# Optimization experiments

Measured on AMD Instinct MI355X. Metric: run time of the kernel, lower is better.

## Reference

```python
import jax, jax.numpy as jnp
import numpy as np

EPS = 1e-5
GROUPS = 16


def _deform_conv_gn(input, offset, mask, weight, bias, gamma, beta):
    # Modulated deformable conv v2 (k=3, stride=1, pad=1) + GroupNorm(16).
    B, C, H, W = input.shape
    Co = weight.shape[0]
    K = 9
    # kernel taps relative to center (pad=1 cancels the -1 origin shift)
    ky = jnp.repeat(jnp.arange(3) - 1, 3).astype(input.dtype)   # [9]
    kx = jnp.tile(jnp.arange(3) - 1, 3).astype(input.dtype)     # [9]
    off = offset.reshape(B, K, 2, H, W)                          # (dy, dx) per tap
    dy, dx = off[:, :, 0], off[:, :, 1]                          # [B,9,H,W]
    y = jnp.arange(H, dtype=input.dtype)[None, None, :, None] + ky[None, :, None, None] + dy
    x = jnp.arange(W, dtype=input.dtype)[None, None, None, :] + kx[None, :, None, None] + dx
    y0 = jnp.floor(y)
    x0 = jnp.floor(x)
    flat = input.reshape(B, C, H * W)

    def corner(yc, xc):
        # zero-padded bilinear corner gather -> [B,C,9,H,W]
        valid = ((yc >= 0) & (yc < H) & (xc >= 0) & (xc < W)).astype(input.dtype)
        yi = jnp.clip(yc, 0, H - 1).astype(jnp.int32)
        xi = jnp.clip(xc, 0, W - 1).astype(jnp.int32)
        idx = (yi * W + xi).reshape(B, -1)
        g = jax.vmap(lambda im, ix: jnp.take(im, ix, axis=1))(flat, idx)
        return g.reshape(B, C, K, H, W) * valid[:, None]

    wy1 = y - y0
    wx1 = x - x0
    wy0 = 1.0 - wy1
    wx0 = 1.0 - wx1
    val = (corner(y0, x0) * (wy0 * wx0)[:, None]
           + corner(y0, x0 + 1.0) * (wy0 * wx1)[:, None]
           + corner(y0 + 1.0, x0) * (wy1 * wx0)[:, None]
           + corner(y0 + 1.0, x0 + 1.0) * (wy1 * wx1)[:, None])
    cols = val * mask[:, None]                                   # modulation [B,C,9,H,W]
    out = jnp.einsum('bckhw,ock->bohw', cols, weight.reshape(Co, C, K))
    out = out + bias[None, :, None, None]
    # GroupNorm(16)
    g = out.reshape(B, GROUPS, Co // GROUPS, H, W)
    mu = g.mean(axis=(2, 3, 4), keepdims=True)
    var = g.var(axis=(2, 3, 4), keepdims=True)
    g = (g - mu) * jax.lax.rsqrt(var + EPS)
    return g.reshape(B, Co, H, W) * gamma[None, :, None, None] + beta[None, :, None, None]


def setup_inputs() -> dict:
    key = jax.random.key(0)
    k1, k2, k3, k4 = jax.random.split(key, 4)
    B, C, Co, H, W = 4, 256, 256, 64, 64
    return {
        'input': jax.random.normal(k1, (B, C, H, W), dtype=jnp.float32),
        'offset': jax.random.normal(k2, (B, 18, H, W), dtype=jnp.float32),
        'mask': jax.random.uniform(k3, (B, 9, H, W), dtype=jnp.float32),
        'weight': jax.random.normal(k4, (Co, C, 3, 3), dtype=jnp.float32) * 0.02,
        'bias': jnp.zeros((Co,), dtype=jnp.float32),
        'gamma': jnp.ones((Co,), dtype=jnp.float32),
        'beta': jnp.zeros((Co,), dtype=jnp.float32),
    }


def reference(input, offset, mask, weight, bias, gamma, beta):
    return _deform_conv_gn(input, offset, mask, weight, bias, gamma, beta)
```

## Files before the change

kernel.cpp:

```cpp
#include <hip/hip_runtime.h>

typedef __attribute__((ext_vector_type(8))) short short8;
typedef __attribute__((ext_vector_type(4))) float f32x4;

#define Bsz 4
#define Cin 256
#define Cout 256
#define Hh 64
#define Ww 64
#define HW 4096
#define NG 16
#define EPSV 1e-5f

#define CSTR 40
#define SPAN 16
#define PLF (SPAN*64)

#define OFF_IN   0
#define SZ_IN    (32 * PLF * 4)
#define OFF_COL  (OFF_IN + SZ_IN)
#define SZ_COL   (2 * 64 * CSTR * 2)
#define OFF_TA   (OFF_COL + SZ_COL)
#define SZ_TA    (576 * 8)
#define OFF_TW   (OFF_TA + SZ_TA)
#define SZ_TW    (576 * 16)
#define OFF_CTL  (OFF_TW + SZ_TW)
#define SMEM_BYTES (OFF_CTL + 16)

static __device__ __forceinline__ unsigned f2bf(float f) {
    unsigned u = __float_as_uint(f);
    return (u + 0x7fffu + ((u >> 16) & 1u)) >> 16;
}

static __device__ __forceinline__ float2 ld8(const float* p) {
    float2 v;
    __builtin_memcpy(&v, p, 8);
    return v;
}

__global__ void wt_kernel(const float* __restrict__ w, ushort* __restrict__ wtb,
                          float* __restrict__ stats) {
    const int i = blockIdx.x * 256 + threadIdx.x;
    if (blockIdx.x == 0 && threadIdx.x < 128) stats[threadIdx.x] = 0.f;
    if (i >= 72 * 256 * 32) return;
    const int cl = i & 31;
    const int o  = (i >> 5) & 255;
    const int ks = i >> 13;
    const int c  = ((ks & 7) << 5) | cl;
    const int kk = ks >> 3;
    wtb[i] = (ushort)f2bf(w[((size_t)o * Cin + c) * 9 + kk]);
}

__launch_bounds__(512, 1)
__global__ void dcn_kernel(const float* __restrict__ in,
                           const float* __restrict__ offs,
                           const float* __restrict__ mask,
                           const ushort* __restrict__ wtb,
                           const float* __restrict__ bias,
                           float* __restrict__ out,
                           float* __restrict__ stats) {
    extern __shared__ char smem[];
    float*  s_in = (float*)(smem + OFF_IN);
    ushort* col  = (ushort*)(smem + OFF_COL);
    int2*   s_ta = (int2*)(smem + OFF_TA);
    float4* s_tw = (float4*)(smem + OFF_TW);
    int*    s_ctl = (int*)(smem + OFF_CTL);

    const int t  = threadIdx.x;
    const int bx = blockIdx.x;
    const int q  = bx & 7, r = bx >> 3;
    const int b  = q >> 1;
    const int h  = ((q & 1) << 5) | r;
    const int lane = t & 63;
    const int wv   = t >> 6;
    const int n    = lane;
    const int quad = lane >> 4;
    const int l15  = lane & 15;

    if (t < 2) s_ctl[t] = (t == 0) ? 64 : -1;
    __syncthreads();

    int my_min = 64, my_max = -1;
    for (int j = t; j < 576; j += 512) {
        const int k = j >> 6, pp = j & 63;
        const float* ob = offs + (size_t)b * 18 * HW + h * Ww + pp;
        const float dy = ob[(2 * k) * HW];
        const float dx = ob[(2 * k + 1) * HW];
        const float m  = mask[((size_t)b * 9 + k) * HW + h * Ww + pp];
        const float y = (float)h + (float)(k / 3 - 1) + dy;
        const float x = (float)pp + (float)(k % 3 - 1) + dx;
        const float y0f = floorf(y), x0f = floorf(x);
        const float ly = y - y0f, lx = x - x0f;
        const float hy = 1.f - ly, hx = 1.f - lx;
        const int y0 = (int)y0f, x0 = (int)x0f;
        const int yc0 = min(max(y0, 0), 63);
        const int yc1 = min(max(y0 + 1, 0), 63);
        const int xb  = min(max(x0, 0), 62);
        float ax = 0.f, ay = 0.f;
        if (x0 == xb) {
            ax = hx;
            ay = lx;
        } else if (x0 < xb) {
            ax = (x0 + 1 == 0) ? lx : 0.f;
        } else {
            ay = (x0 == 63) ? hx : 0.f;
        }
        const float w0 = (y0 >= 0 && y0 < 64) ? m * hy : 0.f;
        const float w1 = (y0 + 1 >= 0 && y0 + 1 < 64) ? m * ly : 0.f;
        s_ta[j] = make_int2(yc0 * 64 + xb, yc1 * 64 + xb);
        s_tw[j] = make_float4(w0 * ax, w0 * ay, w1 * ax, w1 * ay);
        my_min = min(my_min, yc0);
        my_max = max(my_max, yc1);
    }
#pragma unroll
    for (int off = 32; off; off >>= 1) {
        my_min = min(my_min, __shfl_xor(my_min, off));
        my_max = max(my_max, __shfl_xor(my_max, off));
    }
    if (lane == 0) {
        atomicMin(&s_ctl[0], my_min);
        atomicMax(&s_ctl[1], my_max);
    }
    __syncthreads();

    const int ymin = s_ctl[0];
    const bool use_lds = (s_ctl[1] - ymin + 1) <= SPAN;
    const int ymin64 = ymin << 6;

    f32x4 acc[2][4];
#pragma unroll
    for (int i = 0; i < 2; i++)
#pragma unroll
        for (int nt = 0; nt < 4; nt++) acc[i][nt] = (f32x4){0.f, 0.f, 0.f, 0.f};

    const float* inb = in + (size_t)b * Cin * HW;

#define STAGE(cc)                                                              \
    {                                                                          \
        const float* cbs = inb + (size_t)((cc) * 32) * HW;                     \
        _Pragma("unroll")                                                      \
        for (int i = 0; i < 16; i++) {                                         \
            const int g = (wv << 4) | i;                                       \
            const int plane = g >> 2;                                          \
            const int row = min(ymin + ((g & 3) << 2) + (lane >> 4), 63);      \
            const float* src = cbs + (size_t)plane * HW + row * 64 +           \
                               ((lane & 15) << 2);                             \
            __builtin_amdgcn_global_load_lds(                                  \
                (const __attribute__((address_space(1))) void*)src,            \
                (__attribute__((address_space(3))) void*)(smem + OFF_IN +      \
                                                          g * 1024),          \
                16, 0, 0);                                                     \
        }                                                                      \
    }

#define GATHER_L(kk, pk0, pk1)                                             \
    {                                                                      \
        const int2  ad = s_ta[(kk) * 64 + n];                              \
        const float4 tw = s_tw[(kk) * 64 + n];                             \
        const int r0 = ad.x - ymin64, r1 = ad.y - ymin64;                  \
        const float* cb = s_in + (wv << 2) * PLF;                          \
        float vv[4];                                                       \
        _Pragma("unroll")                                                  \
        for (int j = 0; j < 4; j++) {                                      \
            const float* pl = cb + j * PLF;                                \
            const float2 g0 = ld8(pl + r0);                                \
            const float2 g1 = ld8(pl + r1);                                \
            vv[j] = tw.x * g0.x + tw.y * g0.y + tw.z * g1.x + tw.w * g1.y; \
        }                                                                  \
        pk0 = f2bf(vv[0]) | (f2bf(vv[1]) << 16);                           \
        pk1 = f2bf(vv[2]) | (f2bf(vv[3]) << 16);                           \
    }

#define GATHER_G(cc, kk, pk0, pk1)                                         \
    {                                                                      \
        const int2  ad = s_ta[(kk) * 64 + n];                              \
        const float4 tw = s_tw[(kk) * 64 + n];                             \
        const float* cb = inb + (size_t)((cc) * 32 + wv * 4) * HW;         \
        float vv[4];                                                       \
        _Pragma("unroll")                                                  \
        for (int j = 0; j < 4; j++) {                                      \
            const float* pl = cb + j * HW;                                 \
            const float2 g0 = ld8(pl + ad.x);                              \
            const float2 g1 = ld8(pl + ad.y);                              \
            vv[j] = tw.x * g0.x + tw.y * g0.y + tw.z * g1.x + tw.w * g1.y; \
        }                                                                  \
        pk0 = f2bf(vv[0]) | (f2bf(vv[1]) << 16);                           \
        pk1 = f2bf(vv[2]) | (f2bf(vv[3]) << 16);                           \
    }

#define FRAGS_MFMA(ks, p)                                                      \
    {                                                                          \
        const ushort* wp =                                                     \
            wtb + ((size_t)((ks) * 256 + wv * 32 + l15)) * 32 + quad * 8;      \
        const short8 a0 = *(const short8*)wp;                                  \
        const short8 a1 = *(const short8*)(wp + 16 * 32);                      \
        short8 bfr[4];                                                         \
        _Pragma("unroll")                                                      \
        for (int nt = 0; nt < 4; nt++)                                         \
            bfr[nt] = *(const short8*)&col[(p) * (64 * CSTR) +                 \
                                           (nt * 16 + l15) * CSTR + quad * 8]; \
        _Pragma("unroll")                                                      \
        for (int nt = 0; nt < 4; nt++) {                                       \
            acc[0][nt] = __builtin_amdgcn_mfma_f32_16x16x32_bf16(              \
                a0, bfr[nt], acc[0][nt], 0, 0, 0);                             \
            acc[1][nt] = __builtin_amdgcn_mfma_f32_16x16x32_bf16(              \
                a1, bfr[nt], acc[1][nt], 0, 0, 0);                             \
        }                                                                      \
    }

    unsigned pk0, pk1;
    int p = 0;

    if (use_lds) {
        STAGE(0);
        __syncthreads();
        GATHER_L(0, pk0, pk1);
#pragma unroll 1
        for (int s = 0; s < 72; s++) {
            const int cc = s / 9;
            const int kk = s - cc * 9;
            const int ks = kk * 8 + cc;
            *(unsigned long long*)&col[p * (64 * CSTR) + n * CSTR + (wv << 2)] =
                (unsigned long long)pk0 | ((unsigned long long)pk1 << 32);
            __syncthreads();
            const bool bound = (kk == 8) && (s != 71);
            if (bound) {
                STAGE(cc + 1);
            } else if (s != 71) {
                GATHER_L(kk + 1, pk0, pk1);
            }
            FRAGS_MFMA(ks, p);
            if (bound) {
                __syncthreads();
                GATHER_L(0, pk0, pk1);
            }
            p ^= 1;
        }
    } else {
        GATHER_G(0, 0, pk0, pk1);
#pragma unroll 1
        for (int s = 0; s < 72; s++) {
            const int cc = s / 9;
            const int kk = s - cc * 9;
            const int ks = kk * 8 + cc;
            *(unsigned long long*)&col[p * (64 * CSTR) + n * CSTR + (wv << 2)] =
                (unsigned long long)pk0 | ((unsigned long long)pk1 << 32);
            __syncthreads();
            if (s < 71) {
                const int s1 = s + 1;
                const int cc1 = s1 / 9;
                GATHER_G(cc1, s1 - cc1 * 9, pk0, pk1);
            }
            FRAGS_MFMA(ks, p);
            p ^= 1;
        }
    }
#undef STAGE
#undef GATHER_L
#undef GATHER_G
#undef FRAGS_MFMA

    float gs[2], gq[2];
#pragma unroll
    for (int i = 0; i < 2; i++) {
        float s = 0.f, qq = 0.f;
        const int ob = wv * 32 + i * 16 + quad * 4;
#pragma unroll
        for (int reg = 0; reg < 4; reg++) {
            const int o = ob + reg;
            const float bv = bias[o];
            float* op = out + ((size_t)(b * 256 + o)) * HW + h * Ww + l15;
#pragma unroll
            for (int nt = 0; nt < 4; nt++) {
                const float v = acc[i][nt][reg] + bv;
                op[nt * 16] = v;
                s += v;
                qq += v * v;
            }
        }
        gs[i] = s; gq[i] = qq;
    }
#pragma unroll
    for (int off = 32; off; off >>= 1) {
        gs[0] += __shfl_xor(gs[0], off);
        gq[0] += __shfl_xor(gq[0], off);
        gs[1] += __shfl_xor(gs[1], off);
        gq[1] += __shfl_xor(gq[1], off);
    }
    if (lane == 0) {
#pragma unroll
        for (int i = 0; i < 2; i++) {
            const int g = wv * 2 + i;
            atomicAdd(&stats[((size_t)b * NG + g) * 2],     gs[i]);
            atomicAdd(&stats[((size_t)b * NG + g) * 2 + 1], gq[i]);
        }
    }
}

__global__ void gn_apply_kernel(float* __restrict__ x, const float* __restrict__ stats,
                                const float* __restrict__ gamma,
                                const float* __restrict__ beta) {
    const int i = blockIdx.x * 256 + threadIdx.x;
    const int plane = i >> 10;
    const int o = plane & 255;
    const int bg = plane >> 4;
    const float s = stats[bg * 2], q = stats[bg * 2 + 1];
    const float inv_n = 1.f / 65536.f;
    const float mu = s * inv_n;
    const float var = q * inv_n - mu * mu;
    const float rs = rsqrtf(var + EPSV);
    const float ga = gamma[o] * rs;
    const float be = beta[o] - mu * ga;
    float4 v = ((float4*)x)[i];
    v.x = v.x * ga + be;
    v.y = v.y * ga + be;
    v.z = v.z * ga + be;
    v.w = v.w * ga + be;
    ((float4*)x)[i] = v;
}

extern "C" void kernel_launch(void* const* d_in, const int* in_sizes, int n_in,
                              void* d_out, int out_size, void* d_ws, size_t ws_size,
                              hipStream_t stream) {
    const float* input  = (const float*)d_in[0];
    const float* offset = (const float*)d_in[1];
    const float* maskp  = (const float*)d_in[2];
    const float* weight = (const float*)d_in[3];
    const float* bias   = (const float*)d_in[4];
    const float* gamma  = (const float*)d_in[5];
    const float* beta   = (const float*)d_in[6];
    float* out = (float*)d_out;

    ushort* wtb  = (ushort*)d_ws;
    float* stats = (float*)((char*)d_ws + (size_t)Cout * Cin * 9 * sizeof(ushort));

    static int attr_done = 0;
    if (!attr_done) {
        hipFuncSetAttribute((const void*)dcn_kernel,
                            hipFuncAttributeMaxDynamicSharedMemorySize, SMEM_BYTES);
        attr_done = 1;
    }

    hipLaunchKernelGGL(wt_kernel, dim3((Cout * Cin * 9 + 255) / 256), dim3(256), 0,
                       stream, weight, wtb, stats);
    hipLaunchKernelGGL(dcn_kernel, dim3(Bsz * Hh), dim3(512), SMEM_BYTES, stream,
                       input, offset, maskp, wtb, bias, out, stats);
    hipLaunchKernelGGL(gn_apply_kernel, dim3((Bsz * Cout * HW / 4) / 256), dim3(256), 0,
                       stream, out, stats, gamma, beta);
}
```

Measured before the change: 190.8 us.

## Pre-transpose input to channel-pair bf16 rows, split tiles to half-rows for occupancy

A prep kernel converts the input to a bf16 layout with channel pairs interleaved per pixel, stored row-major with channels innermost. The DCN kernel then stages compact rows into LDS and gathers two channels per 4-byte load. Each block now covers half an image row (32 pixels), so twice as many blocks launch with smaller LDS and launch bounds allowing 4 blocks per CU, aiming to raise occupancy and cut LDS and global traffic. In exchange there is an extra transpose pass over the input and a smaller row span (12), so more rows may fall back to the global gather path.

```diff
diff --git a/kernel.cpp b/kernel.cpp
--- a/kernel.cpp
+++ b/kernel.cpp
@@ -13,19 +13,16 @@
 #define EPSV 1e-5f
 
 #define CSTR 40
-#define SPAN 16
-#define PLF (SPAN*64)
+#define SPAN 12
+#define ROWB 4112
 
 #define OFF_IN   0
-#define SZ_IN    (32 * PLF * 4)
-#define OFF_COL  (OFF_IN + SZ_IN)
-#define SZ_COL   (2 * 64 * CSTR * 2)
-#define OFF_TA   (OFF_COL + SZ_COL)
-#define SZ_TA    (576 * 8)
-#define OFF_TW   (OFF_TA + SZ_TA)
-#define SZ_TW    (576 * 16)
-#define OFF_CTL  (OFF_TW + SZ_TW)
-#define SMEM_BYTES (OFF_CTL + 16)
+#define SZ_IN    (SPAN * ROWB)
+#define OFF_COL  49344
+#define OFF_TA   54464
+#define OFF_TW   56768
+#define OFF_CTL  61376
+#define SMEM_BYTES 61392
 
 static __device__ __forceinline__ unsigned f2bf(float f) {
     unsigned u = __float_as_uint(f);
@@ -38,10 +35,33 @@
     return v;
 }
 
-__global__ void wt_kernel(const float* __restrict__ w, ushort* __restrict__ wtb,
-                          float* __restrict__ stats) {
-    const int i = blockIdx.x * 256 + threadIdx.x;
-    if (blockIdx.x == 0 && threadIdx.x < 128) stats[threadIdx.x] = 0.f;
+#define BLO(u) __uint_as_float((u) << 16)
+#define BHI(u) __uint_as_float((u) & 0xffff0000u)
+
+__launch_bounds__(512)
+__global__ void prep_kernel(const float* __restrict__ in,
+                            const float* __restrict__ w,
+                            unsigned* __restrict__ inT,
+                            ushort* __restrict__ wtb,
+                            float* __restrict__ stats) {
+    const int t  = threadIdx.x;
+    const int bx = blockIdx.x;
+    if (bx < 256) {
+        const int b = bx >> 6, y = bx & 63;
+        const int x = t & 63, w8 = t >> 6;
+        const float* src = in + (size_t)b * 256 * HW + y * 64 + x;
+        unsigned* dst = inT + ((size_t)(b * 64 + y) * 128) * 64 + x;
+#pragma unroll
+        for (int it = 0; it < 16; it++) {
+            const int pr = w8 + it * 8;
+            const float a0 = src[(size_t)(2 * pr) * HW];
+            const float a1 = src[(size_t)(2 * pr + 1) * HW];
+            dst[(size_t)pr * 64] = f2bf(a0) | (f2bf(a1) << 16);
+        }
+        return;
+    }
+    if (bx == 256 && t < 128) stats[t] = 0.f;
+    const int i = (bx - 256) * 512 + t;
     if (i >= 72 * 256 * 32) return;
     const int cl = i & 31;
     const int o  = (i >> 5) & 255;
@@ -51,8 +71,9 @@
     wtb[i] = (ushort)f2bf(w[((size_t)o * Cin + c) * 9 + kk]);
 }
 
-__launch_bounds__(512, 1)
+__launch_bounds__(512, 4)
 __global__ void dcn_kernel(const float* __restrict__ in,
+                           const unsigned* __restrict__ inT,
                            const float* __restrict__ offs,
                            const float* __restrict__ mask,
                            const ushort* __restrict__ wtb,
@@ -60,7 +81,6 @@
                            float* __restrict__ out,
                            float* __restrict__ stats) {
     extern __shared__ char smem[];
-    float*  s_in = (float*)(smem + OFF_IN);
     ushort* col  = (ushort*)(smem + OFF_COL);
     int2*   s_ta = (int2*)(smem + OFF_TA);
     float4* s_tw = (float4*)(smem + OFF_TW);
@@ -70,19 +90,23 @@
     const int bx = blockIdx.x;
     const int q  = bx & 7, r = bx >> 3;
     const int b  = q >> 1;
-    const int h  = ((q & 1) << 5) | r;
+    const int h  = ((q & 1) << 5) | (r >> 1);
+    const int wb = (r & 1) << 5;
     const int lane = t & 63;
     const int wv   = t >> 6;
-    const int n    = lane;
     const int quad = lane >> 4;
     const int l15  = lane & 15;
+    const int px   = lane & 31;
+    const int hi   = lane >> 5;
+    const int proff = (2 * wv + hi) * 256;
 
     if (t < 2) s_ctl[t] = (t == 0) ? 64 : -1;
     __syncthreads();
 
     int my_min = 64, my_max = -1;
-    for (int j = t; j < 576; j += 512) {
-        const int k = j >> 6, pp = j & 63;
+    for (int j = t; j < 288; j += 512) {
+        const int k = j >> 5, p = j & 31;
+        const int pp = wb + p;
         const float* ob = offs + (size_t)b * 18 * HW + h * Ww + pp;
         const float dy = ob[(2 * k) * HW];
         const float dx = ob[(2 * k + 1) * HW];
@@ -107,7 +131,7 @@
         }
         const float w0 = (y0 >= 0 && y0 < 64) ? m * hy : 0.f;
         const float w1 = (y0 + 1 >= 0 && y0 + 1 < 64) ? m * ly : 0.f;
-        s_ta[j] = make_int2(yc0 * 64 + xb, yc1 * 64 + xb);
+        s_ta[j] = make_int2(yc0 * ROWB + xb * 4, yc1 * ROWB + xb * 4);
         s_tw[j] = make_float4(w0 * ax, w0 * ay, w1 * ax, w1 * ay);
         my_min = min(my_min, yc0);
         my_max = max(my_max, yc1);
@@ -125,67 +149,69 @@
 
     const int ymin = s_ctl[0];
     const bool use_lds = (s_ctl[1] - ymin + 1) <= SPAN;
-    const int ymin64 = ymin << 6;
-
-    f32x4 acc[2][4];
+    const int ybase = ymin * ROWB;
+
+    f32x4 acc[2][2];
 #pragma unroll
     for (int i = 0; i < 2; i++)
 #pragma unroll
-        for (int nt = 0; nt < 4; nt++) acc[i][nt] = (f32x4){0.f, 0.f, 0.f, 0.f};
+        for (int nt = 0; nt < 2; nt++) acc[i][nt] = (f32x4){0.f, 0.f, 0.f, 0.f};
 
     const float* inb = in + (size_t)b * Cin * HW;
 
 #define STAGE(cc)                                                              \
     {                                                                          \
-        const float* cbs = inb + (size_t)((cc) * 32) * HW;                     \
         _Pragma("unroll")                                                      \
-        for (int i = 0; i < 16; i++) {                                         \
-            const int g = (wv << 4) | i;                                       \
-            const int plane = g >> 2;                                          \
-            const int row = min(ymin + ((g & 3) << 2) + (lane >> 4), 63);      \
-            const float* src = cbs + (size_t)plane * HW + row * 64 +           \
-                               ((lane & 15) << 2);                             \
+        for (int i = 0; i < 6; i++) {                                          \
+            const int g = wv * 6 + i;                                          \
+            const int rr = g >> 2, seg = g & 3;                                \
+            const int row = min(ymin + rr, 63);                                \
+            const unsigned* src = inT +                                        \
+                ((size_t)(b * 64 + row) * 128 + (cc) * 16) * 64 +              \
+                seg * 256 + lane * 4;                                          \
             __builtin_amdgcn_global_load_lds(                                  \
                 (const __attribute__((address_space(1))) void*)src,            \
                 (__attribute__((address_space(3))) void*)(smem + OFF_IN +      \
-                                                          g * 1024),          \
+                    rr * ROWB + seg * 1024),                                   \
                 16, 0, 0);                                                     \
         }                                                                      \
     }
 
-#define GATHER_L(kk, pk0, pk1)                                             \
+#define GATHER_L(kk, pk)                                                   \
     {                                                                      \
-        const int2  ad = s_ta[(kk) * 64 + n];                              \
-        const float4 tw = s_tw[(kk) * 64 + n];                             \
-        const int r0 = ad.x - ymin64, r1 = ad.y - ymin64;                  \
-        const float* cb = s_in + (wv << 2) * PLF;                          \
-        float vv[4];                                                       \
+        const int2  ad = s_ta[(kk) * 32 + px];                             \
+        const float4 tw = s_tw[(kk) * 32 + px];                            \
+        const char* bp = smem + OFF_IN + proff - ybase;                    \
+        const float2 f0 = ld8((const float*)(bp + ad.x));                  \
+        const float2 f1 = ld8((const float*)(bp + ad.y));                  \
+        const unsigned u00 = __float_as_uint(f0.x);                        \
+        const unsigned u01 = __float_as_uint(f0.y);                        \
+        const unsigned u10 = __float_as_uint(f1.x);                        \
+        const unsigned u11 = __float_as_uint(f1.y);                        \
+        const float v0 = tw.x * BLO(u00) + tw.y * BLO(u01) +               \
+                         tw.z * BLO(u10) + tw.w * BLO(u11);                \
+        const float v1 = tw.x * BHI(u00) + tw.y * BHI(u01) +               \
+                         tw.z * BHI(u10) + tw.w * BHI(u11);                \
+        pk = f2bf(v0) | (f2bf(v1) << 16);                                  \
+    }
+
+#define GATHER_G(cc, kk, pk)                                               \
+    {                                                                      \
+        const int2  ad = s_ta[(kk) * 32 + px];                             \
+        const float4 tw = s_tw[(kk) * 32 + px];                            \
+        const int y0r = ad.x / ROWB, x0r = (ad.x - y0r * ROWB) >> 2;       \
+        const int y1r = ad.y / ROWB, x1r = (ad.y - y1r * ROWB) >> 2;       \
+        const int adx = y0r * 64 + x0r, ady = y1r * 64 + x1r;              \
+        const float* cb = inb + (size_t)((cc) * 32 + wv * 4 + hi * 2) * HW;\
+        float vv[2];                                                       \
         _Pragma("unroll")                                                  \
-        for (int j = 0; j < 4; j++) {                                      \
-            const float* pl = cb + j * PLF;                                \
-            const float2 g0 = ld8(pl + r0);                                \
-            const float2 g1 = ld8(pl + r1);                                \
+        for (int j = 0; j < 2; j++) {                                      \
+            const float* pl = cb + j * HW;                                 \
+            const float2 g0 = ld8(pl + adx);                               \
+            const float2 g1 = ld8(pl + ady);                               \
             vv[j] = tw.x * g0.x + tw.y * g0.y + tw.z * g1.x + tw.w * g1.y; \
         }                                                                  \
-        pk0 = f2bf(vv[0]) | (f2bf(vv[1]) << 16);                           \
-        pk1 = f2bf(vv[2]) | (f2bf(vv[3]) << 16);                           \
-    }
-
-#define GATHER_G(cc, kk, pk0, pk1)                                         \
-    {                                                                      \
-        const int2  ad = s_ta[(kk) * 64 + n];                              \
-        const float4 tw = s_tw[(kk) * 64 + n];                             \
-        const float* cb = inb + (size_t)((cc) * 32 + wv * 4) * HW;         \
-        float vv[4];                                                       \
-        _Pragma("unroll")                                                  \
-        for (int j = 0; j < 4; j++) {                                      \
-            const float* pl = cb + j * HW;                                 \
-            const float2 g0 = ld8(pl + ad.x);                              \
-            const float2 g1 = ld8(pl + ad.y);                              \
-            vv[j] = tw.x * g0.x + tw.y * g0.y + tw.z * g1.x + tw.w * g1.y; \
-        }                                                                  \
-        pk0 = f2bf(vv[0]) | (f2bf(vv[1]) << 16);                           \
-        pk1 = f2bf(vv[2]) | (f2bf(vv[3]) << 16);                           \
+        pk = f2bf(vv[0]) | (f2bf(vv[1]) << 16);                           \
     }
 
 #define FRAGS_MFMA(ks, p)                                                      \
@@ -194,13 +220,13 @@
             wtb + ((size_t)((ks) * 256 + wv * 32 + l15)) * 32 + quad * 8;      \
         const short8 a0 = *(const short8*)wp;                                  \
         const short8 a1 = *(const short8*)(wp + 16 * 32);                      \
-        short8 bfr[4];                                                         \
+        short8 bfr[2];                                                         \
         _Pragma("unroll")                                                      \
-        for (int nt = 0; nt < 4; nt++)                                         \
-            bfr[nt] = *(const short8*)&col[(p) * (64 * CSTR) +                 \
+        for (int nt = 0; nt < 2; nt++)                                         \
+            bfr[nt] = *(const short8*)&col[(p) * (32 * CSTR) +                 \
                                            (nt * 16 + l15) * CSTR + quad * 8]; \
         _Pragma("unroll")                                                      \
-        for (int nt = 0; nt < 4; nt++) {                                       \
+        for (int nt = 0; nt < 2; nt++) {                                       \
             acc[0][nt] = __builtin_amdgcn_mfma_f32_16x16x32_bf16(              \
                 a0, bfr[nt], acc[0][nt], 0, 0, 0);                             \
             acc[1][nt] = __builtin_amdgcn_mfma_f32_16x16x32_bf16(              \
@@ -208,48 +234,46 @@
         }                                                                      \
     }
 
-    unsigned pk0, pk1;
+    unsigned pk;
     int p = 0;
 
     if (use_lds) {
         STAGE(0);
         __syncthreads();
-        GATHER_L(0, pk0, pk1);
+        GATHER_L(0, pk);
 #pragma unroll 1
         for (int s = 0; s < 72; s++) {
             const int cc = s / 9;
             const int kk = s - cc * 9;
             const int ks = kk * 8 + cc;
-            *(unsigned long long*)&col[p * (64 * CSTR) + n * CSTR + (wv << 2)] =
-                (unsigned long long)pk0 | ((unsigned long long)pk1 << 32);
+            *(unsigned*)&col[p * (32 * CSTR) + px * CSTR + (wv << 2) + (hi << 1)] = pk;
             __syncthreads();
             const bool bound = (kk == 8) && (s != 71);
             if (bound) {
                 STAGE(cc + 1);
             } else if (s != 71) {
-                GATHER_L(kk + 1, pk0, pk1);
+                GATHER_L(kk + 1, pk);
             }
             FRAGS_MFMA(ks, p);
             if (bound) {
                 __syncthreads();
-                GATHER_L(0, pk0, pk1);
+                GATHER_L(0, pk);
             }
             p ^= 1;
         }
     } else {
-        GATHER_G(0, 0, pk0, pk1);
+        GATHER_G(0, 0, pk);
 #pragma unroll 1
         for (int s = 0; s < 72; s++) {
             const int cc = s / 9;
             const int kk = s - cc * 9;
             const int ks = kk * 8 + cc;
-            *(unsigned long long*)&col[p * (64 * CSTR) + n * CSTR + (wv << 2)] =
-                (unsigned long long)pk0 | ((unsigned long long)pk1 << 32);
+            *(unsigned*)&col[p * (32 * CSTR) + px * CSTR + (wv << 2) + (hi << 1)] = pk;
             __syncthreads();
             if (s < 71) {
                 const int s1 = s + 1;
                 const int cc1 = s1 / 9;
-                GATHER_G(cc1, s1 - cc1 * 9, pk0, pk1);
+                GATHER_G(cc1, s1 - cc1 * 9, pk);
             }
             FRAGS_MFMA(ks, p);
             p ^= 1;
@@ -269,9 +293,9 @@
         for (int reg = 0; reg < 4; reg++) {
             const int o = ob + reg;
             const float bv = bias[o];
-            float* op = out + ((size_t)(b * 256 + o)) * HW + h * Ww + l15;
-#pragma unroll
-            for (int nt = 0; nt < 4; nt++) {
+            float* op = out + ((size_t)(b * 256 + o)) * HW + h * Ww + wb + l15;
+#pragma unroll
+            for (int nt = 0; nt < 2; nt++) {
                 const float v = acc[i][nt][reg] + bv;
                 op[nt * 16] = v;
                 s += v;
@@ -333,6 +357,7 @@
 
     ushort* wtb  = (ushort*)d_ws;
     float* stats = (float*)((char*)d_ws + (size_t)Cout * Cin * 9 * sizeof(ushort));
+    unsigned* inT = (unsigned*)((char*)d_ws + 1180160);
 
     static int attr_done = 0;
     if (!attr_done) {
@@ -341,10 +366,10 @@
         attr_done = 1;
     }
 
-    hipLaunchKernelGGL(wt_kernel, dim3((Cout * Cin * 9 + 255) / 256), dim3(256), 0,
-                       stream, weight, wtb, stats);
-    hipLaunchKernelGGL(dcn_kernel, dim3(Bsz * Hh), dim3(512), SMEM_BYTES, stream,
-                       input, offset, maskp, wtb, bias, out, stats);
+    hipLaunchKernelGGL(prep_kernel, dim3(256 + 1152), dim3(512), 0, stream,
+                       input, weight, inT, wtb, stats);
+    hipLaunchKernelGGL(dcn_kernel, dim3(Bsz * Hh * 2), dim3(512), SMEM_BYTES, stream,
+                       input, inT, offset, maskp, wtb, bias, out, stats);
     hipLaunchKernelGGL(gn_apply_kernel, dim3((Bsz * Cout * HW / 4) / 256), dim3(256), 0,
                        stream, out, stats, gamma, beta);
 }
```

Result: slower. 206.2 us (+8.1%).
